# Kernel tuning notes

Measured on AMD Instinct MI355X. Metric: run time of the kernel, lower is better.

## Reference

```python
import jax, jax.numpy as jnp
import numpy as np

NUM_RADIAL = 7
EDGE_DIM = 128
PAIR_CUTOFF = 6.0
THREE_CUTOFF = 4.0
ENV_P = 8  # envelope exponent
N_UND = 500_000
N_DIR = 2 * N_UND
LN_EPS = 1e-5


def bessel_expansion(r, cutoff):
    """CHGNet-style radial Bessel basis with smooth polynomial envelope.
    r: [E] -> [E, NUM_RADIAL]"""
    p = float(ENV_P)
    x = r / cutoff  # [E]
    env = (1.0
           - (p + 1.0) * (p + 2.0) / 2.0 * x ** p
           + p * (p + 2.0) * x ** (p + 1.0)
           - p * (p + 1.0) / 2.0 * x ** (p + 2.0))
    env = jnp.where(x < 1.0, env, 0.0)  # [E]
    freq = jnp.pi * jnp.arange(1, NUM_RADIAL + 1, dtype=r.dtype)  # [R]
    norm = jnp.sqrt(2.0 / cutoff).astype(r.dtype)
    # sin(n*pi*r/cutoff)/r * envelope
    basis = norm * jnp.sin(freq[None, :] * x[:, None]) / r[:, None]
    return basis * env[:, None]


def setup_inputs() -> dict:
    key = jax.random.key(0)
    k1, k2, k3, k4 = jax.random.split(key, 4)
    # edge lengths in [0.5, 6.0) to stay physical and avoid 1/r blowup
    edge_lengths = 0.5 + 5.5 * jax.random.uniform(k1, (N_DIR,), dtype=jnp.float32)
    # each undirected edge u owns directed edges (2u, 2u+1)
    undirected2directed = 2 * jnp.arange(N_UND, dtype=jnp.int64 if jax.config.jax_enable_x64 else jnp.int32)
    directed2undirected = jnp.repeat(jnp.arange(N_UND, dtype=undirected2directed.dtype), 2)
    s1 = 1.0 / np.sqrt(NUM_RADIAL)
    s2 = 1.0 / np.sqrt(EDGE_DIM)
    W1 = jax.random.normal(k2, (EDGE_DIM, NUM_RADIAL), dtype=jnp.float32) * s1
    W2 = jax.random.normal(k3, (EDGE_DIM, EDGE_DIM), dtype=jnp.float32) * s2
    W_swish = jax.random.normal(k4, (EDGE_DIM, EDGE_DIM), dtype=jnp.float32) * s2
    ln_gamma = jnp.ones((EDGE_DIM,), dtype=jnp.float32)
    ln_beta = jnp.zeros((EDGE_DIM,), dtype=jnp.float32)
    return {
        "edge_lengths": edge_lengths,
        "undirected2directed": undirected2directed,
        "directed2undirected": directed2undirected,
        "W1": W1,
        "W2": W2,
        "ln_gamma": ln_gamma,
        "ln_beta": ln_beta,
        "W_swish": W_swish,
    }


def reference(edge_lengths, undirected2directed, directed2undirected,
              W1, W2, ln_gamma, ln_beta, W_swish):
    n_und = undirected2directed.shape[0]
    # gather unique (undirected) edge lengths
    uel = jnp.take(edge_lengths, undirected2directed, axis=0)  # [U]
    pairwise_rbf = bessel_expansion(uel, PAIR_CUTOFF)   # [U, R]
    threebody_rbf = bessel_expansion(uel, THREE_CUTOFF)  # [U, R]
    # linear1 on undirected features
    feat_u = pairwise_rbf @ W1.T  # [U, D]
    # broadcast to directed edges, linear2
    feat_d = jnp.take(feat_u, directed2undirected, axis=0) @ W2.T  # [E, D]
    # LayerNorm over feature dim
    mu = jnp.mean(feat_d, axis=-1, keepdims=True)
    var = jnp.mean(jnp.square(feat_d - mu), axis=-1, keepdims=True)
    feat_d = (feat_d - mu) * jax.lax.rsqrt(var + LN_EPS) * ln_gamma + ln_beta
    # segment mean back to undirected edges
    seg_sum = jax.ops.segment_sum(feat_d, directed2undirected, num_segments=n_und)
    counts = jax.ops.segment_sum(jnp.ones((feat_d.shape[0],), feat_d.dtype),
                                 directed2undirected, num_segments=n_und)
    edge_feat = seg_sum / jnp.maximum(counts, 1.0)[:, None]
    # swish layer: linear (no bias) + SiLU
    edge_feat = jax.nn.silu(edge_feat @ W_swish.T)  # [U, D]
    return edge_feat, pairwise_rbf, threebody_rbf
```

## Files before the change

kernel.cpp:

```cpp
#include <hip/hip_runtime.h>
#include <math.h>

#define NR 7
#define ED 128
#define NUND 500000


__global__ __launch_bounds__(128) void precompute_kernel(
    const float* __restrict__ W1, const float* __restrict__ W2,
    const float* __restrict__ gamma, const float* __restrict__ beta,
    const float* __restrict__ Wsw, float* __restrict__ ws)
{
  __shared__ float sW12[ED][NR];
  const int d = threadIdx.x;
  float w12[NR];
#pragma unroll
  for (int k = 0; k < NR; ++k) w12[k] = 0.f;
  for (int j = 0; j < ED; ++j) {
    float w2 = W2[d * ED + j];
#pragma unroll
    for (int k = 0; k < NR; ++k) w12[k] = fmaf(w2, W1[j * NR + k], w12[k]);
  }
#pragma unroll
  for (int k = 0; k < NR; ++k) sW12[d][k] = w12[k];
  __syncthreads();

  float m[NR];
#pragma unroll
  for (int k = 0; k < NR; ++k) m[k] = 0.f;
  float wsum = 0.f, bb = 0.f;
  for (int j = 0; j < ED; ++j) {
    float wv = Wsw[d * ED + j];
    float wg = wv * gamma[j];
    wsum += wg;
    bb = fmaf(wv, beta[j], bb);
#pragma unroll
    for (int k = 0; k < NR; ++k) m[k] = fmaf(wg, sW12[j][k], m[k]);
  }
#pragma unroll
  for (int k = 0; k < NR; ++k) ws[d * NR + k] = m[k];
  ws[896 + d] = wsum;
  ws[1024 + d] = bb;

  if (d < 49) {
    int k = d / 7, k2 = d % 7;
    float q = 0.f;
    for (int j = 0; j < ED; ++j) q = fmaf(sW12[j][k], sW12[j][k2], q);
    ws[1152 + d] = q;
  } else if (d < 56) {
    int k = d - 49;
    float s = 0.f;
    for (int j = 0; j < ED; ++j) s += sW12[j][k];
    ws[1201 + k] = s * (1.f / 128.f);
  }
}

__global__ __launch_bounds__(256) void edge_kernel(
    const float* __restrict__ el, const int* __restrict__ u2d,
    const float* __restrict__ ws, float* __restrict__ out)
{
  __shared__ float sQ[56];
  __shared__ float sA[256][8];
  const int t = threadIdx.x;

  if (t < 56) sQ[t] = ws[1152 + t];

  const int l = t & 31;
  const int g = t >> 5;
  float M4[4][NR], ws4[4], bb4[4];
#pragma unroll
  for (int c = 0; c < 4; ++c) {
    int d = 4 * l + c;
#pragma unroll
    for (int k = 0; k < NR; ++k) M4[c][k] = ws[d * NR + k];
    ws4[c] = ws[896 + d];
    bb4[c] = ws[1024 + d];
  }

  const int u0 = blockIdx.x * 256;
  const int u  = u0 + t;
  __syncthreads();

  if (u < NUND) {
    const float r = el[u2d[u]];
    const float invr = 1.f / r;
    const float PI = 3.14159265358979323846f;

    float rb[NR];
    {
      float x = r * (1.f / 6.f);
      float x2 = x * x, x4 = x2 * x2, x8 = x4 * x4;
      float env = fmaf(x8, fmaf(x, fmaf(x, -36.f, 80.f), -45.f), 1.f);
      if (x >= 1.f) env = 0.f;
      float sc = 0.57735026918962576f * env * invr;
      float a = PI * x;
      float s1, c1;
      __sincosf(a, &s1, &c1);
      float twoc = 2.f * c1;
      float sm1 = 0.f, s = s1;
#pragma unroll
      for (int k = 0; k < NR; ++k) {
        rb[k] = sc * s;
        float nxt = fmaf(twoc, s, -sm1);
        sm1 = s; s = nxt;
      }
      float* op = out + (size_t)64000000 + (size_t)u * 7;
#pragma unroll
      for (int k = 0; k < NR; ++k) op[k] = rb[k];
    }
    {
      float x = r * 0.25f;
      float x2 = x * x, x4 = x2 * x2, x8 = x4 * x4;
      float env = fmaf(x8, fmaf(x, fmaf(x, -36.f, 80.f), -45.f), 1.f);
      if (x >= 1.f) env = 0.f;
      float sc = 0.70710678118654752f * env * invr;
      float a = PI * x;
      float s1, c1;
      __sincosf(a, &s1, &c1);
      float twoc = 2.f * c1;
      float sm1 = 0.f, s = s1;
      float* op = out + (size_t)67500000 + (size_t)u * 7;
#pragma unroll
      for (int k = 0; k < NR; ++k) {
        op[k] = sc * s;
        float nxt = fmaf(twoc, s, -sm1);
        sm1 = s; s = nxt;
      }
    }
    float mu = 0.f;
#pragma unroll
    for (int k = 0; k < NR; ++k) mu = fmaf(rb[k], sQ[49 + k], mu);
    float msq = 0.f;
#pragma unroll
    for (int k = 0; k < NR; ++k) {
      float acc = 0.f;
#pragma unroll
      for (int k2 = 0; k2 < NR; ++k2) acc = fmaf(sQ[k * 7 + k2], rb[k2], acc);
      msq = fmaf(rb[k], acc, msq);
    }
    float var = fmaf(msq, (1.f / 128.f), -mu * mu);
    float rs = rsqrtf(var + 1e-5f);
#pragma unroll
    for (int k = 0; k < NR; ++k) sA[t][k] = rb[k] * rs;
    sA[t][7] = mu * rs;
  } else {
#pragma unroll
    for (int k = 0; k < 8; ++k) sA[t][k] = 0.f;
  }
  __syncthreads();

  const int nv = (NUND - u0 < 256) ? (NUND - u0) : 256;
  for (int eb = 0; eb < 256; eb += 8) {
    int e = eb + g;
    if (e < nv) {
      float4 v0 = *(const float4*)&sA[e][0];
      float4 v1 = *(const float4*)&sA[e][4];
      float4 res;
      float* rp = &res.x;
#pragma unroll
      for (int c = 0; c < 4; ++c) {
        float pre = fmaf(-v1.w, ws4[c], bb4[c]);
        pre = fmaf(v0.x, M4[c][0], pre);
        pre = fmaf(v0.y, M4[c][1], pre);
        pre = fmaf(v0.z, M4[c][2], pre);
        pre = fmaf(v0.w, M4[c][3], pre);
        pre = fmaf(v1.x, M4[c][4], pre);
        pre = fmaf(v1.y, M4[c][5], pre);
        pre = fmaf(v1.z, M4[c][6], pre);
        float sig = 1.f / (1.f + __expf(-pre));
        rp[c] = pre * sig;
      }
      *(float4*)&out[(size_t)(u0 + e) * 128 + 4 * l] = res;
    }
  }
}

extern "C" void kernel_launch(void* const* d_in, const int* in_sizes, int n_in,
                              void* d_out, int out_size, void* d_ws, size_t ws_size,
                              hipStream_t stream) {
  const float* edge_lengths = (const float*)d_in[0];
  const int*   u2d          = (const int*)d_in[1];
  const float* W1    = (const float*)d_in[3];
  const float* W2    = (const float*)d_in[4];
  const float* gamma = (const float*)d_in[5];
  const float* beta  = (const float*)d_in[6];
  const float* Wsw   = (const float*)d_in[7];
  float* out = (float*)d_out;
  float* ws  = (float*)d_ws;

  hipLaunchKernelGGL(precompute_kernel, dim3(1), dim3(128), 0, stream,
                     W1, W2, gamma, beta, Wsw, ws);
  const int nblk = (NUND + 255) / 256;
  hipLaunchKernelGGL(edge_kernel, dim3(nblk), dim3(256), 0, stream,
                     edge_lengths, u2d, ws, out);
}
```

Baseline: 329.8 us.

## Coalesce RBF output stores via shared staging and parallelize weight precompute

The edge kernel now stages both radial basis outputs in shared memory and writes them to global memory in contiguous per-block runs, instead of each thread writing seven strided floats. The single-block precompute kernel now uses 1024 threads, loads W2 and W_swish into padded shared memory, and spreads the reductions across threads. This targets uncoalesced stores in the main kernel and the serial latency of the weight precompute, at the cost of extra shared memory and barriers per block.

```diff
diff --git a/kernel.cpp b/kernel.cpp
--- a/kernel.cpp
+++ b/kernel.cpp
@@ -4,54 +4,75 @@
 #define NR 7
 #define ED 128
 #define NUND 500000
-
-
-__global__ __launch_bounds__(128) void precompute_kernel(
+#define PITCH 132
+
+
+__global__ __launch_bounds__(1024) void precompute_kernel(
     const float* __restrict__ W1, const float* __restrict__ W2,
     const float* __restrict__ gamma, const float* __restrict__ beta,
     const float* __restrict__ Wsw, float* __restrict__ ws)
 {
-  __shared__ float sW12[ED][NR];
-  const int d = threadIdx.x;
-  float w12[NR];
-#pragma unroll
-  for (int k = 0; k < NR; ++k) w12[k] = 0.f;
-  for (int j = 0; j < ED; ++j) {
-    float w2 = W2[d * ED + j];
-#pragma unroll
-    for (int k = 0; k < NR; ++k) w12[k] = fmaf(w2, W1[j * NR + k], w12[k]);
-  }
-#pragma unroll
-  for (int k = 0; k < NR; ++k) sW12[d][k] = w12[k];
-  __syncthreads();
-
-  float m[NR];
-#pragma unroll
-  for (int k = 0; k < NR; ++k) m[k] = 0.f;
-  float wsum = 0.f, bb = 0.f;
-  for (int j = 0; j < ED; ++j) {
-    float wv = Wsw[d * ED + j];
-    float wg = wv * gamma[j];
-    wsum += wg;
-    bb = fmaf(wv, beta[j], bb);
-#pragma unroll
-    for (int k = 0; k < NR; ++k) m[k] = fmaf(wg, sW12[j][k], m[k]);
-  }
-#pragma unroll
-  for (int k = 0; k < NR; ++k) ws[d * NR + k] = m[k];
-  ws[896 + d] = wsum;
-  ws[1024 + d] = bb;
-
-  if (d < 49) {
-    int k = d / 7, k2 = d % 7;
+  __shared__ float sBig[ED * PITCH];
+  __shared__ float sW1[ED * NR];
+  __shared__ float sW12[ED * NR];
+  __shared__ float sGB[2 * ED];
+  const int t = threadIdx.x;
+
+  for (int i = t; i < ED * NR; i += 1024) sW1[i] = W1[i];
+  if (t < ED) { sGB[t] = gamma[t]; sGB[ED + t] = beta[t]; }
+  {
+    const float4* src = (const float4*)W2;
+    for (int i = t; i < ED * ED / 4; i += 1024) {
+      int row = i >> 5, c4 = i & 31;
+      *(float4*)&sBig[row * PITCH + 4 * c4] = src[i];
+    }
+  }
+  __syncthreads();
+
+  const int d = t >> 3, k = t & 7;
+  if (k < NR) {
+    float acc = 0.f;
+    for (int j = 0; j < ED; ++j)
+      acc = fmaf(sBig[d * PITCH + j], sW1[j * NR + k], acc);
+    sW12[d * NR + k] = acc;
+  }
+  __syncthreads();
+
+  if (t < 49) {
+    int a = t / 7, b = t % 7;
     float q = 0.f;
-    for (int j = 0; j < ED; ++j) q = fmaf(sW12[j][k], sW12[j][k2], q);
-    ws[1152 + d] = q;
-  } else if (d < 56) {
-    int k = d - 49;
+    for (int j = 0; j < ED; ++j) q = fmaf(sW12[j * NR + a], sW12[j * NR + b], q);
+    ws[1152 + t] = q;
+  } else if (t < 56) {
+    int a = t - 49;
     float s = 0.f;
-    for (int j = 0; j < ED; ++j) s += sW12[j][k];
-    ws[1201 + k] = s * (1.f / 128.f);
+    for (int j = 0; j < ED; ++j) s += sW12[j * NR + a];
+    ws[1201 + a] = s * (1.f / 128.f);
+  }
+
+  {
+    const float4* src = (const float4*)Wsw;
+    for (int i = t; i < ED * ED / 4; i += 1024) {
+      int row = i >> 5, c4 = i & 31;
+      *(float4*)&sBig[row * PITCH + 4 * c4] = src[i];
+    }
+  }
+  __syncthreads();
+
+  if (k < NR) {
+    float m = 0.f;
+    for (int j = 0; j < ED; ++j)
+      m = fmaf(sGB[j] * sBig[d * PITCH + j], sW12[j * NR + k], m);
+    ws[d * NR + k] = m;
+  } else {
+    float wsum = 0.f, bb = 0.f;
+    for (int j = 0; j < ED; ++j) {
+      float wv = sBig[d * PITCH + j];
+      wsum = fmaf(wv, sGB[j], wsum);
+      bb   = fmaf(wv, sGB[ED + j], bb);
+    }
+    ws[896 + d] = wsum;
+    ws[1024 + d] = bb;
   }
 }
 
@@ -61,6 +82,7 @@
 {
   __shared__ float sQ[56];
   __shared__ float sA[256][8];
+  __shared__ float sB[256][8];
   const int t = threadIdx.x;
 
   if (t < 56) sQ[t] = ws[1152 + t];
@@ -79,14 +101,16 @@
 
   const int u0 = blockIdx.x * 256;
   const int u  = u0 + t;
-  __syncthreads();
-
+  const int nv = (NUND - u0 < 256) ? (NUND - u0) : 256;
+  __syncthreads();
+
+  float rs = 0.f, mu = 0.f;
+  float rb[NR];
   if (u < NUND) {
     const float r = el[u2d[u]];
     const float invr = 1.f / r;
     const float PI = 3.14159265358979323846f;
 
-    float rb[NR];
     {
       float x = r * (1.f / 6.f);
       float x2 = x * x, x4 = x2 * x2, x8 = x4 * x4;
@@ -101,12 +125,10 @@
 #pragma unroll
       for (int k = 0; k < NR; ++k) {
         rb[k] = sc * s;
+        sA[t][k] = rb[k];
         float nxt = fmaf(twoc, s, -sm1);
         sm1 = s; s = nxt;
       }
-      float* op = out + (size_t)64000000 + (size_t)u * 7;
-#pragma unroll
-      for (int k = 0; k < NR; ++k) op[k] = rb[k];
     }
     {
       float x = r * 0.25f;
@@ -119,15 +141,13 @@
       __sincosf(a, &s1, &c1);
       float twoc = 2.f * c1;
       float sm1 = 0.f, s = s1;
-      float* op = out + (size_t)67500000 + (size_t)u * 7;
 #pragma unroll
       for (int k = 0; k < NR; ++k) {
-        op[k] = sc * s;
+        sB[t][k] = sc * s;
         float nxt = fmaf(twoc, s, -sm1);
         sm1 = s; s = nxt;
       }
     }
-    float mu = 0.f;
 #pragma unroll
     for (int k = 0; k < NR; ++k) mu = fmaf(rb[k], sQ[49 + k], mu);
     float msq = 0.f;
@@ -139,17 +159,29 @@
       msq = fmaf(rb[k], acc, msq);
     }
     float var = fmaf(msq, (1.f / 128.f), -mu * mu);
-    float rs = rsqrtf(var + 1e-5f);
+    rs = rsqrtf(var + 1e-5f);
+  }
+  __syncthreads();
+
+  {
+    float* outP = out + (size_t)64000000 + (size_t)u0 * 7;
+    float* outT = out + (size_t)67500000 + (size_t)u0 * 7;
+    const int total = nv * 7;
+    for (int s = t; s < total; s += 256) {
+      int e = s / 7, c = s - 7 * e;
+      outP[s] = sA[e][c];
+      outT[s] = sB[e][c];
+    }
+  }
+  __syncthreads();
+
+  if (u < NUND) {
 #pragma unroll
     for (int k = 0; k < NR; ++k) sA[t][k] = rb[k] * rs;
     sA[t][7] = mu * rs;
-  } else {
-#pragma unroll
-    for (int k = 0; k < 8; ++k) sA[t][k] = 0.f;
-  }
-  __syncthreads();
-
-  const int nv = (NUND - u0 < 256) ? (NUND - u0) : 256;
+  }
+  __syncthreads();
+
   for (int eb = 0; eb < 256; eb += 8) {
     int e = eb + g;
     if (e < nv) {
@@ -188,7 +220,7 @@
   float* out = (float*)d_out;
   float* ws  = (float*)d_ws;
 
-  hipLaunchKernelGGL(precompute_kernel, dim3(1), dim3(128), 0, stream,
+  hipLaunchKernelGGL(precompute_kernel, dim3(1), dim3(1024), 0, stream,
                      W1, W2, gamma, beta, Wsw, ws);
   const int nblk = (NUND + 255) / 256;
   hipLaunchKernelGGL(edge_kernel, dim3(nblk), dim3(256), 0, stream,
```

Measured after the change: 319.0 us. 1.03x faster.
